# Optimization experiments

Measured on AMD Instinct MI355X. Metric: run time of the kernel, lower is better.

The kernel has to match this reference:

```python
import jax, jax.numpy as jnp
import numpy as np

B, T, D, H, L, K, DFF = 8, 512, 512, 8, 4, 31, 2048
DK = D // H
PAD = (K - 1) // 2

def _ln(x, g, b, eps=1e-5):
    m = x.mean(-1, keepdims=True)
    v = ((x - m) ** 2).mean(-1, keepdims=True)
    return (x - m) * jax.lax.rsqrt(v + eps) * g + b

def _swish(x):
    return x * jax.nn.sigmoid(x)

def _rel_shift(x):
    # x: [B,H,T,P] with P = 2T-1 (Transformer-XL style shift)
    b, h, q, p = x.shape
    x = jnp.pad(x, ((0, 0), (0, 0), (0, 0), (1, 0)))
    x = x.reshape(b, h, p + 1, q)[:, :, 1:].reshape(b, h, q, p)
    return x

def setup_inputs() -> dict:
    key = jax.random.key(0)
    ks = iter(jax.random.split(key, 64))
    def w(shape, s=0.02):
        return jax.random.normal(next(ks), shape, jnp.float32) * s
    inp = {
        'x': jax.random.normal(next(ks), (B, T, D), jnp.float32),
        'pos_emb': jax.random.normal(next(ks), (1, 2 * T - 1, D), jnp.float32),
        'ln1_g': jnp.ones((L, D)), 'ln1_b': jnp.zeros((L, D)),
        'ff1_w1': w((L, D, DFF)), 'ff1_b1': jnp.zeros((L, DFF)),
        'ff1_w2': w((L, DFF, D)), 'ff1_b2': jnp.zeros((L, D)),
        'lnA_g': jnp.ones((L, D)), 'lnA_b': jnp.zeros((L, D)),
        'Wq': w((L, D, D)), 'bq': jnp.zeros((L, D)),
        'Wk': w((L, D, D)), 'bk': jnp.zeros((L, D)),
        'Wv': w((L, D, D)), 'bv': jnp.zeros((L, D)),
        'Wo': w((L, D, D)), 'bo': jnp.zeros((L, D)),
        'Wpos': w((L, D, D)),
        'pbu': jnp.zeros((L, H, DK)), 'pbv': jnp.zeros((L, H, DK)),
        'lnC_g': jnp.ones((L, D)), 'lnC_b': jnp.zeros((L, D)),
        'pw1_w': w((L, 2 * D, D)), 'pw1_b': jnp.zeros((L, 2 * D)),
        'dw_w': w((L, D, K)), 'dw_b': jnp.zeros((L, D)),
        'cln_g': jnp.ones((L, D)), 'cln_b': jnp.zeros((L, D)),
        'pw2_w': w((L, D, D)), 'pw2_b': jnp.zeros((L, D)),
        'ln2_g': jnp.ones((L, D)), 'ln2_b': jnp.zeros((L, D)),
        'ff2_w1': w((L, D, DFF)), 'ff2_b1': jnp.zeros((L, DFF)),
        'ff2_w2': w((L, DFF, D)), 'ff2_b2': jnp.zeros((L, D)),
        'lnO_g': jnp.ones((L, D)), 'lnO_b': jnp.zeros((L, D)),
    }
    return inp

def reference(x, pos_emb, ln1_g, ln1_b, ff1_w1, ff1_b1, ff1_w2, ff1_b2,
              lnA_g, lnA_b, Wq, bq, Wk, bk, Wv, bv, Wo, bo, Wpos, pbu, pbv,
              lnC_g, lnC_b, pw1_w, pw1_b, dw_w, dw_b, cln_g, cln_b, pw2_w, pw2_b,
              ln2_g, ln2_b, ff2_w1, ff2_b1, ff2_w2, ff2_b2, lnO_g, lnO_b):
    scale = 1.0 / np.sqrt(DK).astype(np.float32)
    for i in range(L):
        # FFN 1 (half-step residual)
        res = x
        y = _ln(x, ln1_g[i], ln1_b[i])
        y = _swish(y @ ff1_w1[i] + ff1_b1[i]) @ ff1_w2[i] + ff1_b2[i]
        res = res + 0.5 * y
        # rel-pos multi-head self-attention
        y = _ln(res, lnA_g[i], lnA_b[i])
        q = (y @ Wq[i] + bq[i]).reshape(B, T, H, DK)
        k = (y @ Wk[i] + bk[i]).reshape(B, T, H, DK)
        v = (y @ Wv[i] + bv[i]).reshape(B, T, H, DK)
        p = (pos_emb @ Wpos[i]).reshape(1, 2 * T - 1, H, DK)
        ac = jnp.einsum('bthd,bshd->bhts', q + pbu[i], k)          # content score
        bd = jnp.einsum('bthd,xshd->bhts', q + pbv[i], p)          # position score
        bd = _rel_shift(bd)[..., :T]
        attn = jax.nn.softmax((ac + bd) * scale, axis=-1)
        o = jnp.einsum('bhts,bshd->bthd', attn, v).reshape(B, T, D)
        res = res + (o @ Wo[i] + bo[i])
        # convolution module
        y = _ln(res, lnC_g[i], lnC_b[i])
        y = y @ pw1_w[i].T + pw1_b[i]                               # (B,T,2D)
        a, g = jnp.split(y, 2, axis=-1)
        y = a * jax.nn.sigmoid(g)                                   # GLU over channels
        y = jax.lax.conv_general_dilated(
            y.transpose(0, 2, 1), dw_w[i][:, None, :],
            window_strides=(1,), padding=[(PAD, PAD)],
            feature_group_count=D,
            dimension_numbers=('NCH', 'OIH', 'NCH'))
        y = y.transpose(0, 2, 1) + dw_b[i]                          # (B,T,D)
        y = _swish(_ln(y, cln_g[i], cln_b[i]))
        y = y @ pw2_w[i].T + pw2_b[i]
        res = res + y
        # FFN 2 (half-step residual)
        y = _ln(res, ln2_g[i], ln2_b[i])
        y = _swish(y @ ff2_w1[i] + ff2_b1[i]) @ ff2_w2[i] + ff2_b2[i]
        res = res + 0.5 * y
        x = _ln(res, lnO_g[i], lnO_b[i])
    return x
```

## Files before the change

kernel.cpp:

```cpp
#include <hip/hip_runtime.h>


typedef unsigned short u16;
typedef unsigned int u32;
typedef __attribute__((ext_vector_type(8))) short bf16x8;
typedef __attribute__((ext_vector_type(4))) float f32x4;

#define DI __device__ __forceinline__

constexpr int CT = 512;
constexpr int CD = 512;
constexpr int CH = 8;
constexpr int CDK = 64;
constexpr int CDFF = 2048;
constexpr int CNBT = 4096;
constexpr int CL = 4;

DI u16 f2bf(float f) {
  u32 u = __builtin_bit_cast(u32, f);
  u = u + 0x7fffu + ((u >> 16) & 1u);
  return (u16)(u >> 16);
}
DI float bf2f(u16 h) { u32 u = ((u32)h) << 16; return __builtin_bit_cast(float, u); }
DI u32 pack2(float a, float b) { return (u32)f2bf(a) | ((u32)f2bf(b) << 16); }
DI float sigm(float x) { return 1.0f / (1.0f + __expf(-x)); }

DI f32x4 MFMA(bf16x8 a, bf16x8 b, f32x4 c) {
  return __builtin_amdgcn_mfma_f32_16x16x32_bf16(a, b, c, 0, 0, 0);
}

DI void gload16(const void* g, void* l) {
  __builtin_amdgcn_global_load_lds((const __attribute__((address_space(1))) void*)g,
                                   (__attribute__((address_space(3))) void*)l, 16, 0, 0);
}

DI float wsum(float v) {
#pragma unroll
  for (int o = 32; o > 0; o >>= 1) v += __shfl_xor(v, o, 64);
  return v;
}

__global__ __launch_bounds__(256) void tconv_k(const float* __restrict__ in,
                                               u16* __restrict__ out, int R, int C,
                                               long inZ, long outZ) {
  __shared__ float t[32][33];
  int c0 = blockIdx.x * 32, r0 = blockIdx.y * 32;
  const float* ip = in + (long)blockIdx.z * inZ;
  u16* op = out + (long)blockIdx.z * outZ;
#pragma unroll
  for (int i = threadIdx.y; i < 32; i += 8)
    t[i][threadIdx.x] = ip[(long)(r0 + i) * C + c0 + threadIdx.x];
  __syncthreads();
#pragma unroll
  for (int i = threadIdx.y; i < 32; i += 8)
    op[(long)(c0 + i) * R + r0 + threadIdx.x] = f2bf(t[threadIdx.x][i]);
}

__global__ __launch_bounds__(256) void cvt_k(const float* __restrict__ in,
                                             u16* __restrict__ out, long nIn, long nOut,
                                             long inZ, long outZ) {
  long i = ((long)blockIdx.x * 256 + threadIdx.x) * 4;
  if (i >= nOut) return;
  const float* ip = in + (long)blockIdx.y * inZ;
  u16* op = out + (long)blockIdx.y * outZ;
  u16 o[4];
#pragma unroll
  for (int j = 0; j < 4; ++j) {
    long idx = i + j;
    o[j] = (idx < nIn) ? f2bf(ip[idx]) : (u16)0;
  }
  uint2 st;
  st.x = (u32)o[0] | ((u32)o[1] << 16);
  st.y = (u32)o[2] | ((u32)o[3] << 16);
  *(uint2*)&op[i] = st;
}

__global__ __launch_bounds__(256) void pwperm_k(const float* __restrict__ in,
                                                u16* __restrict__ out) {
  int l = blockIdx.y;
  long i = (long)blockIdx.x * 256 + threadIdx.x;
  long n = i >> 7;
  int c = (int)(i & 127) * 4;
  int q = (int)(n >> 4) & 1;
  long r = (q ? 512 : 0) + ((n >> 5) << 4) + (n & 15);
  const float* ip = in + ((long)l * 1024 + r) * 512 + c;
  float4 v = *(const float4*)ip;
  u16* op = out + ((long)l * 1024 + n) * 512 + c;
  uint2 st;
  st.x = pack2(v.x, v.y);
  st.y = pack2(v.z, v.w);
  *(uint2*)op = st;
}

__global__ __launch_bounds__(256) void dwt_k(const float* __restrict__ in,
                                             float* __restrict__ out) {
  int l = blockIdx.y;
  int idx = blockIdx.x * 256 + threadIdx.x;
  if (idx >= 512 * 31) return;
  int k = idx >> 9, d = idx & 511;
  out[(long)l * 31 * 512 + idx] = in[(long)l * 512 * 31 + d * 31 + k];
}

__global__ __launch_bounds__(256) void qkvbias_k(const float* __restrict__ bq,
                                                 const float* __restrict__ bk,
                                                 const float* __restrict__ bv,
                                                 float* __restrict__ out) {
  int z = blockIdx.y;
  int j = blockIdx.x * 256 + threadIdx.x;
  float v;
  if (j < 512) v = bq[z * 512 + j];
  else if (j < 1024) v = bk[z * 512 + j - 512];
  else v = bv[z * 512 + j - 1024];
  out[z * 1536 + j] = v;
}

__global__ __launch_bounds__(256) void copy_k(const float* __restrict__ in,
                                              float* __restrict__ out) {
  long i = ((long)blockIdx.x * 256 + threadIdx.x) * 4;
  *(float4*)(out + i) = *(const float4*)(in + i);
}

template <int F32OUT>
__global__ __launch_bounds__(256) void ln_k(const float* in, void* out,
                                            const float* gw, const float* bw) {
  int tid = threadIdx.x, wid = tid >> 6, lane = tid & 63;
  long row = (long)blockIdx.x * 4 + wid;
  const float* x = in + row * CD + lane * 8;
  float4 v0 = *(const float4*)x;
  float4 v1 = *(const float4*)(x + 4);
  float s = v0.x + v0.y + v0.z + v0.w + v1.x + v1.y + v1.z + v1.w;
  float q = v0.x * v0.x + v0.y * v0.y + v0.z * v0.z + v0.w * v0.w +
            v1.x * v1.x + v1.y * v1.y + v1.z * v1.z + v1.w * v1.w;
  s = wsum(s);
  q = wsum(q);
  float mean = s * (1.0f / CD);
  float var = q * (1.0f / CD) - mean * mean;
  float rs = rsqrtf(var + 1e-5f);
  int c = lane * 8;
  float4 g0 = *(const float4*)(gw + c), g1 = *(const float4*)(gw + c + 4);
  float4 b0 = *(const float4*)(bw + c), b1 = *(const float4*)(bw + c + 4);
  float y0 = (v0.x - mean) * rs * g0.x + b0.x;
  float y1 = (v0.y - mean) * rs * g0.y + b0.y;
  float y2 = (v0.z - mean) * rs * g0.z + b0.z;
  float y3 = (v0.w - mean) * rs * g0.w + b0.w;
  float y4 = (v1.x - mean) * rs * g1.x + b1.x;
  float y5 = (v1.y - mean) * rs * g1.y + b1.y;
  float y6 = (v1.z - mean) * rs * g1.z + b1.z;
  float y7 = (v1.w - mean) * rs * g1.w + b1.w;
  if (F32OUT) {
    float* o = (float*)out + row * CD + c;
    *(float4*)o = make_float4(y0, y1, y2, y3);
    *(float4*)(o + 4) = make_float4(y4, y5, y6, y7);
  } else {
    u16* o = (u16*)out + row * CD + c;
    uint4 pk;
    pk.x = pack2(y0, y1);
    pk.y = pack2(y2, y3);
    pk.z = pack2(y4, y5);
    pk.w = pack2(y6, y7);
    *(uint4*)o = pk;
  }
}

template <int EPI, int SPLITK>
__global__ __launch_bounds__(256, 2) void gemm2_k(
    const u16* __restrict__ A, const u16* __restrict__ B, void* C,
    const float* __restrict__ bias, float alpha, int lda, int ldb, int ldc, int Kd) {
  __shared__ u16 lds[2][2][64 * 64];
  const int tid = threadIdx.x, wid = tid >> 6, lane = tid & 63;
  const int m0 = blockIdx.x * 64, n0 = blockIdx.y * 64;
  const int wm = wid >> 1, wn = wid & 1;
  const int fr = lane & 15, fq = lane >> 4;
  const f32x4 vz = {0.f, 0.f, 0.f, 0.f};
  f32x4 acc[2][2] = {{vz, vz}, {vz, vz}};

  const int Kc = Kd / SPLITK;
  const int kb0 = (SPLITK > 1) ? blockIdx.z * Kc : 0;
  const int nK = Kc / 64;

  auto stage = [&](int buf, int kt) {
    const int k0 = kb0 + kt * 64;
#pragma unroll
    for (int r = 0; r < 2; ++r) {
      int bi = r * 4096 + tid * 16;
      int row = bi >> 7;
      int ch = ((bi >> 4) & 7) ^ (row & 7);
      gload16(A + (long)(m0 + row) * lda + k0 + ch * 8,
              (char*)&lds[buf][0][0] + r * 4096 + wid * 1024);
      gload16(B + (long)(n0 + row) * ldb + k0 + ch * 8,
              (char*)&lds[buf][1][0] + r * 4096 + wid * 1024);
    }
  };

  stage(0, 0);
  asm volatile("s_waitcnt vmcnt(0)" ::: "memory");
  __syncthreads();
  int buf = 0;
  for (int kt = 0; kt < nK; ++kt) {
    if (kt + 1 < nK) stage(buf ^ 1, kt + 1);
    bf16x8 af[2][2], bfv[2][2];
#pragma unroll
    for (int ks = 0; ks < 2; ++ks) {
      int ch = ks * 4 + fq;
#pragma unroll
      for (int i = 0; i < 2; ++i) {
        int arow = wm * 32 + i * 16 + fr;
        af[ks][i] = *(const bf16x8*)((const char*)&lds[buf][0][0] + arow * 128 +
                                     ((ch ^ (arow & 7)) << 4));
        int brow = wn * 32 + i * 16 + fr;
        bfv[ks][i] = *(const bf16x8*)((const char*)&lds[buf][1][0] + brow * 128 +
                                      ((ch ^ (brow & 7)) << 4));
      }
    }
#pragma unroll
    for (int ks = 0; ks < 2; ++ks)
#pragma unroll
      for (int mi = 0; mi < 2; ++mi)
#pragma unroll
        for (int ni = 0; ni < 2; ++ni)
          acc[mi][ni] = MFMA(af[ks][mi], bfv[ks][ni], acc[mi][ni]);
    asm volatile("s_waitcnt vmcnt(0)" ::: "memory");
    __syncthreads();
    buf ^= 1;
  }

  if constexpr (EPI == 7) {
    const int ucol = (n0 >> 1) + wn * 16 + fr;
    float ba = bias[ucol], bg = bias[512 + ucol];
#pragma unroll
    for (int mi = 0; mi < 2; ++mi) {
      const int gmB = m0 + wm * 32 + mi * 16 + fq * 4;
#pragma unroll
      for (int r = 0; r < 4; ++r) {
        float va = acc[mi][0][r] + ba;
        float vg = acc[mi][1][r] + bg;
        ((u16*)C)[(long)(gmB + r) * 512 + ucol] = f2bf(va * sigm(vg));
      }
    }
  } else {
#pragma unroll
    for (int mi = 0; mi < 2; ++mi) {
      const int gmB = m0 + wm * 32 + mi * 16 + fq * 4;
#pragma unroll
      for (int ni = 0; ni < 2; ++ni) {
        const int gn = n0 + wn * 32 + ni * 16 + fr;
        float bv_ = 0.f;
        if constexpr (EPI == 1 || EPI == 2 || EPI == 3) bv_ = bias[gn];
#pragma unroll
        for (int r = 0; r < 4; ++r) {
          const int gm = gmB + r;
          float v = acc[mi][ni][r];
          long idx = (long)gm * ldc + gn;
          if constexpr (EPI == 0) ((u16*)C)[idx] = f2bf(v);
          else if constexpr (EPI == 1) ((u16*)C)[idx] = f2bf(v + bv_);
          else if constexpr (EPI == 2) {
            float x = v + bv_;
            ((u16*)C)[idx] = f2bf(x * sigm(x));
          } else if constexpr (EPI == 3) {
            float* R = (float*)C;
            if constexpr (SPLITK > 1) {
              float add = alpha * (v + (blockIdx.z == 0 ? bv_ : 0.f));
              atomicAdd(&R[idx], add);
            } else {
              R[idx] += alpha * (v + bv_);
            }
          }
        }
      }
    }
  }
}

__global__ __launch_bounds__(256) void vtrans_k(const u16* __restrict__ qkv,
                                                u16* __restrict__ vt) {
  __shared__ u16 t[64][80];
  int tid = threadIdx.x;
  int t0 = blockIdx.x * 64;
  int bh = blockIdx.y, b = bh >> 3, h = bh & 7;
  {
    int tl = tid >> 2, dg = (tid & 3) * 16;
    const u16* src = qkv + ((long)(b * CT + t0 + tl)) * 1536 + 1024 + h * 64 + dg;
    uint4 a0 = *(const uint4*)src;
    uint4 a1 = *(const uint4*)(src + 8);
    *(uint4*)&t[tl][dg] = a0;
    *(uint4*)&t[tl][dg + 8] = a1;
  }
  __syncthreads();
  {
    int dl = tid >> 2, tg = (tid & 3) * 16;
    u16* dst = vt + ((long)bh * 64 + dl) * CT + t0 + tg;
    u16 tmp[16];
#pragma unroll
    for (int j = 0; j < 16; ++j) tmp[j] = t[tg + j][dl];
    uint4 o0, o1;
    o0.x = (u32)tmp[0] | ((u32)tmp[1] << 16);
    o0.y = (u32)tmp[2] | ((u32)tmp[3] << 16);
    o0.z = (u32)tmp[4] | ((u32)tmp[5] << 16);
    o0.w = (u32)tmp[6] | ((u32)tmp[7] << 16);
    o1.x = (u32)tmp[8] | ((u32)tmp[9] << 16);
    o1.y = (u32)tmp[10] | ((u32)tmp[11] << 16);
    o1.z = (u32)tmp[12] | ((u32)tmp[13] << 16);
    o1.w = (u32)tmp[14] | ((u32)tmp[15] << 16);
    *(uint4*)dst = o0;
    *(uint4*)(dst + 8) = o1;
  }
}

__global__ __launch_bounds__(256, 2) void attn_k(
    const u16* __restrict__ qkvp, const u16* __restrict__ pball,
    const float* __restrict__ pbuL, const float* __restrict__ pbvL,
    const u16* __restrict__ vt, u16* __restrict__ out) {
  __shared__ u16 ldsK[2][64 * 64];
  __shared__ u16 ldsP[2][128 * 64];
  __shared__ u16 bd0s[4][16 * 80];
  __shared__ u16 stile[4][16 * 64];
  const int tid = threadIdx.x, wid = tid >> 6, lane = tid & 63;
  const int t0 = blockIdx.x * 64;
  const int bh = blockIdx.y, b = bh >> 3, h = bh & 7;
  const int fr = lane & 15, fq = lane >> 4;

  const u16* kbase = qkvp + (long)(b * CT) * 1536 + 512 + h * 64;
  const u16* pbase = pball + h * 64;
  const float* pu = pbuL + h * 64;
  const float* pv = pbvL + h * 64;

  const u16* qp = qkvp + (long)(b * CT + t0 + wid * 16 + fr) * 1536 + h * 64;
  bf16x8 qua[2], qva[2];
#pragma unroll
  for (int kk = 0; kk < 2; ++kk) {
    bf16x8 qw = *(const bf16x8*)(qp + kk * 32 + fq * 8);
    const float* bu = pu + kk * 32 + fq * 8;
    const float* bv = pv + kk * 32 + fq * 8;
#pragma unroll
    for (int j = 0; j < 8; ++j) {
      float qf = bf2f((u16)qw[j]);
      qua[kk][j] = (short)f2bf(qf + bu[j]);
      qva[kk][j] = (short)f2bf(qf + bv[j]);
    }
  }

  const f32x4 vz = {0.f, 0.f, 0.f, 0.f};
  f32x4 oacc[4] = {vz, vz, vz, vz};
  float m_run[4] = {-1e30f, -1e30f, -1e30f, -1e30f};
  float l_run[4] = {0.f, 0.f, 0.f, 0.f};
  const int jbw = (3 - wid) * 16;

  auto stage = [&](int buf, int st) {
    int s0 = st * 64, j0 = s0 - t0 + 448;
#pragma unroll
    for (int r = 0; r < 2; ++r) {
      int c = r * 256 + tid;
      int row = c >> 3, cs = (c & 7) ^ (row & 7);
      gload16(kbase + (long)(s0 + row) * 1536 + cs * 8,
              (char*)&ldsK[buf][0] + r * 4096 + wid * 1024);
    }
#pragma unroll
    for (int r = 0; r < 4; ++r) {
      int c = r * 256 + tid;
      int row = c >> 3, cs = (c & 7) ^ (row & 7);
      gload16(pbase + (long)(j0 + row) * 2048 + cs * 8,
              (char*)&ldsP[buf][0] + r * 4096 + wid * 1024);
    }
  };

  stage(0, 0);
  int cur = 0;
  for (int st = 0; st < 8; ++st) {
    const int s0 = st * 64;
    if (st + 1 < 8) {
      stage(cur ^ 1, st + 1);
      asm volatile("s_waitcnt vmcnt(6)" ::: "memory");
    } else {
      asm volatile("s_waitcnt vmcnt(0)" ::: "memory");
    }
    __syncthreads();

    bf16x8 vb[4][2];
#pragma unroll
    for (int ni = 0; ni < 4; ++ni)
#pragma unroll
      for (int kk = 0; kk < 2; ++kk)
        vb[ni][kk] = *(const bf16x8*)&vt[((long)bh * 64 + ni * 16 + fr) * 512 +
                                         s0 + kk * 32 + fq * 8];

    f32x4 ac[4] = {vz, vz, vz, vz};
#pragma unroll
    for (int kk = 0; kk < 2; ++kk) {
#pragma unroll
      for (int ni = 0; ni < 4; ++ni) {
        int row = ni * 16 + fr;
        bf16x8 kb = *(const bf16x8*)((const char*)&ldsK[cur][0] +
                                     ((row * 128 + kk * 64 + fq * 16) ^ ((row & 7) << 4)));
        ac[ni] = MFMA(qua[kk], kb, ac[ni]);
      }
    }
    f32x4 bd[5] = {vz, vz, vz, vz, vz};
#pragma unroll
    for (int kk = 0; kk < 2; ++kk) {
#pragma unroll
      for (int nbi = 0; nbi < 5; ++nbi) {
        int row = jbw + nbi * 16 + fr;
        bf16x8 pb = *(const bf16x8*)((const char*)&ldsP[cur][0] +
                                     ((row * 128 + kk * 64 + fq * 16) ^ ((row & 7) << 4)));
        bd[nbi] = MFMA(qva[kk], pb, bd[nbi]);
      }
    }
#pragma unroll
    for (int nbi = 0; nbi < 5; ++nbi)
#pragma unroll
      for (int r = 0; r < 4; ++r)
        bd0s[wid][(fq * 4 + r) * 80 + nbi * 16 + fr] = f2bf(bd[nbi][r]);

    float vals[4][4];
#pragma unroll
    for (int ni = 0; ni < 4; ++ni)
#pragma unroll
      for (int r = 0; r < 4; ++r) {
        int tlw = fq * 4 + r;
        int jcol = ni * 16 + fr + 15 - tlw;
        vals[ni][r] = (ac[ni][r] + bf2f(bd0s[wid][tlw * 80 + jcol])) * 0.125f;
      }
    float scf[4];
#pragma unroll
    for (int r = 0; r < 4; ++r) {
      float mx = fmaxf(fmaxf(vals[0][r], vals[1][r]), fmaxf(vals[2][r], vals[3][r]));
      mx = fmaxf(mx, __shfl_xor(mx, 1));
      mx = fmaxf(mx, __shfl_xor(mx, 2));
      mx = fmaxf(mx, __shfl_xor(mx, 4));
      mx = fmaxf(mx, __shfl_xor(mx, 8));
      float mnew = fmaxf(m_run[r], mx);
      scf[r] = __expf(m_run[r] - mnew);
      m_run[r] = mnew;
      float sum = 0.f;
#pragma unroll
      for (int ni = 0; ni < 4; ++ni) {
        float p = __expf(vals[ni][r] - mnew);
        vals[ni][r] = p;
        sum += p;
      }
      sum += __shfl_xor(sum, 1);
      sum += __shfl_xor(sum, 2);
      sum += __shfl_xor(sum, 4);
      sum += __shfl_xor(sum, 8);
      l_run[r] = l_run[r] * scf[r] + sum;
    }
#pragma unroll
    for (int ni = 0; ni < 4; ++ni)
#pragma unroll
      for (int r = 0; r < 4; ++r) {
        int tlw = fq * 4 + r;
        *(u16*)((char*)&stile[wid][0] +
                (((tlw * 128) + (ni * 16 + fr) * 2) ^ ((tlw & 7) << 4))) =
            f2bf(vals[ni][r]);
      }
#pragma unroll
    for (int ni = 0; ni < 4; ++ni)
#pragma unroll
      for (int r = 0; r < 4; ++r) oacc[ni][r] *= scf[r];
#pragma unroll
    for (int kk = 0; kk < 2; ++kk) {
      bf16x8 pa = *(const bf16x8*)((const char*)&stile[wid][0] +
                                   ((fr * 128 + kk * 64 + fq * 16) ^ ((fr & 7) << 4)));
#pragma unroll
      for (int ni = 0; ni < 4; ++ni) oacc[ni] = MFMA(pa, vb[ni][kk], oacc[ni]);
    }
    __syncthreads();
    cur ^= 1;
  }

  float inv[4];
#pragma unroll
  for (int r = 0; r < 4; ++r) inv[r] = 1.0f / l_run[r];
#pragma unroll
  for (int ni = 0; ni < 4; ++ni)
#pragma unroll
    for (int r = 0; r < 4; ++r) {
      long row = (long)(b * CT + t0 + wid * 16 + fq * 4 + r) * CD + h * CDK;
      out[row + ni * 16 + fr] = f2bf(oacc[ni][r] * inv[r]);
    }
}

__global__ __launch_bounds__(256) void conv2_k(const u16* __restrict__ u,
                                               const float* __restrict__ wT,
                                               const float* __restrict__ wb,
                                               const float* __restrict__ cg,
                                               const float* __restrict__ cb,
                                               u16* __restrict__ out) {
  constexpr int TT = 8;
  int tid = threadIdx.x, d0 = tid * 2;
  int b = blockIdx.y, t0 = blockIdx.x * TT;
  const u16* ub = u + ((long)b * CT) * CD + d0;

  u32 strip[TT + 30];
#pragma unroll
  for (int j = 0; j < TT + 30; ++j) {
    int tt = t0 + j - 15;
    strip[j] = ((unsigned)tt < (unsigned)CT) ? *(const u32*)(ub + (long)tt * CD) : 0u;
  }
  float2 bias = *(const float2*)(wb + d0);
  float a0[TT], a1[TT];
#pragma unroll
  for (int t = 0; t < TT; ++t) { a0[t] = bias.x; a1[t] = bias.y; }
#pragma unroll
  for (int k = 0; k < 31; ++k) {
    float2 wk = *(const float2*)(wT + k * CD + d0);
#pragma unroll
    for (int t = 0; t < TT; ++t) {
      u32 pr = strip[t + k];
      a0[t] += bf2f((u16)(pr & 0xffff)) * wk.x;
      a1[t] += bf2f((u16)(pr >> 16)) * wk.y;
    }
  }
  __shared__ float redS[4][TT], redQ[4][TT];
  int wid = tid >> 6, lane = tid & 63;
#pragma unroll
  for (int t = 0; t < TT; ++t) {
    float s = a0[t] + a1[t];
    float q = a0[t] * a0[t] + a1[t] * a1[t];
    s = wsum(s);
    q = wsum(q);
    if (lane == 0) { redS[wid][t] = s; redQ[wid][t] = q; }
  }
  __syncthreads();
  float2 g2 = *(const float2*)(cg + d0);
  float2 b2 = *(const float2*)(cb + d0);
#pragma unroll
  for (int t = 0; t < TT; ++t) {
    float s = redS[0][t] + redS[1][t] + redS[2][t] + redS[3][t];
    float q = redQ[0][t] + redQ[1][t] + redQ[2][t] + redQ[3][t];
    float mean = s * (1.f / 512), var = q * (1.f / 512) - mean * mean;
    float rs = rsqrtf(var + 1e-5f);
    float y0 = (a0[t] - mean) * rs * g2.x + b2.x;
    float y1 = (a1[t] - mean) * rs * g2.y + b2.y;
    y0 = y0 * sigm(y0);
    y1 = y1 * sigm(y1);
    *(u32*)(out + ((long)(b * CT + t0 + t)) * CD + d0) = pack2(y0, y1);
  }
}

extern "C" void kernel_launch(void* const* d_in, const int* in_sizes, int n_in,
                              void* d_out, int out_size, void* d_ws, size_t ws_size,
                              hipStream_t stream) {
  const float* in_x   = (const float*)d_in[0];
  const float* in_pos = (const float*)d_in[1];
  const float* ln1_g  = (const float*)d_in[2];
  const float* ln1_b  = (const float*)d_in[3];
  const float* ff1_w1 = (const float*)d_in[4];
  const float* ff1_b1 = (const float*)d_in[5];
  const float* ff1_w2 = (const float*)d_in[6];
  const float* ff1_b2 = (const float*)d_in[7];
  const float* lnA_g  = (const float*)d_in[8];
  const float* lnA_b  = (const float*)d_in[9];
  const float* Wq     = (const float*)d_in[10];
  const float* bq     = (const float*)d_in[11];
  const float* Wk     = (const float*)d_in[12];
  const float* bk     = (const float*)d_in[13];
  const float* Wv     = (const float*)d_in[14];
  const float* bv     = (const float*)d_in[15];
  const float* Wo     = (const float*)d_in[16];
  const float* bo     = (const float*)d_in[17];
  const float* Wpos   = (const float*)d_in[18];
  const float* pbu    = (const float*)d_in[19];
  const float* pbv    = (const float*)d_in[20];
  const float* lnC_g  = (const float*)d_in[21];
  const float* lnC_b  = (const float*)d_in[22];
  const float* pw1_w  = (const float*)d_in[23];
  const float* pw1_b  = (const float*)d_in[24];
  const float* dw_w   = (const float*)d_in[25];
  const float* dw_b   = (const float*)d_in[26];
  const float* cln_g  = (const float*)d_in[27];
  const float* cln_b  = (const float*)d_in[28];
  const float* pw2_w  = (const float*)d_in[29];
  const float* pw2_b  = (const float*)d_in[30];
  const float* ln2_g  = (const float*)d_in[31];
  const float* ln2_b  = (const float*)d_in[32];
  const float* ff2_w1 = (const float*)d_in[33];
  const float* ff2_b1 = (const float*)d_in[34];
  const float* ff2_w2 = (const float*)d_in[35];
  const float* ff2_b2 = (const float*)d_in[36];
  const float* lnO_g  = (const float*)d_in[37];
  const float* lnO_b  = (const float*)d_in[38];
  (void)in_sizes; (void)n_in; (void)out_size; (void)ws_size;

  char* ws = (char*)d_ws;
  size_t off = 0;
  auto alloc = [&](size_t bytes) -> void* {
    off = (off + 255) & ~(size_t)255;
    void* p = ws + off;
    off += bytes;
    return p;
  };

  u16* wt_ff1w1 = (u16*)alloc((size_t)CL * CDFF * CD * 2);
  u16* wt_ff1w2 = (u16*)alloc((size_t)CL * CD * CDFF * 2);
  u16* wt_qkv   = (u16*)alloc((size_t)CL * 1536 * CD * 2);
  u16* wt_o     = (u16*)alloc((size_t)CL * CD * CD * 2);
  u16* wt_pos   = (u16*)alloc((size_t)CL * CD * CD * 2);
  u16* w_pw1p   = (u16*)alloc((size_t)CL * 1024 * CD * 2);
  u16* w_pw2    = (u16*)alloc((size_t)CL * CD * CD * 2);
  u16* wt_ff2w1 = (u16*)alloc((size_t)CL * CDFF * CD * 2);
  u16* wt_ff2w2 = (u16*)alloc((size_t)CL * CD * CDFF * 2);
  float* qkvbias = (float*)alloc((size_t)CL * 1536 * 4);
  u16* posbf = (u16*)alloc((size_t)1024 * CD * 2);
  float* dwT = (float*)alloc((size_t)CL * 31 * CD * 4);
  u16* pbf_all = (u16*)alloc((size_t)1024 * 2048 * 2);
  float* cur = (float*)alloc((size_t)CNBT * CD * 4);
  u16* ybf   = (u16*)alloc((size_t)CNBT * CD * 2);
  u16* qkv   = (u16*)alloc((size_t)CNBT * 1536 * 2);
  u16* hbf   = (u16*)alloc((size_t)CNBT * CDFF * 2);
  u16* vt    = (u16*)alloc((size_t)64 * CDK * CT * 2);
  u16* obf   = (u16*)alloc((size_t)CNBT * CD * 2);
  u16* ubuf  = (u16*)alloc((size_t)CNBT * CD * 2);
  u16* cbf   = (u16*)alloc((size_t)CNBT * CD * 2);

  dim3 b256(256);
  dim3 tb(32, 8);

  tconv_k<<<dim3(CDFF / 32, CD / 32, CL), tb, 0, stream>>>(ff1_w1, wt_ff1w1, CD, CDFF,
                                                           (long)CD * CDFF, (long)CDFF * CD);
  tconv_k<<<dim3(CD / 32, CDFF / 32, CL), tb, 0, stream>>>(ff1_w2, wt_ff1w2, CDFF, CD,
                                                           (long)CDFF * CD, (long)CD * CDFF);
  tconv_k<<<dim3(CD / 32, CD / 32, CL), tb, 0, stream>>>(Wq, wt_qkv, CD, CD,
                                                         (long)CD * CD, 1536L * CD);
  tconv_k<<<dim3(CD / 32, CD / 32, CL), tb, 0, stream>>>(Wk, wt_qkv + 512 * 512, CD, CD,
                                                         (long)CD * CD, 1536L * CD);
  tconv_k<<<dim3(CD / 32, CD / 32, CL), tb, 0, stream>>>(Wv, wt_qkv + 1024 * 512, CD, CD,
                                                         (long)CD * CD, 1536L * CD);
  tconv_k<<<dim3(CD / 32, CD / 32, CL), tb, 0, stream>>>(Wo, wt_o, CD, CD,
                                                         (long)CD * CD, (long)CD * CD);
  tconv_k<<<dim3(CD / 32, CD / 32, CL), tb, 0, stream>>>(Wpos, wt_pos, CD, CD,
                                                         (long)CD * CD, (long)CD * CD);
  tconv_k<<<dim3(CDFF / 32, CD / 32, CL), tb, 0, stream>>>(ff2_w1, wt_ff2w1, CD, CDFF,
                                                           (long)CD * CDFF, (long)CDFF * CD);
  tconv_k<<<dim3(CD / 32, CDFF / 32, CL), tb, 0, stream>>>(ff2_w2, wt_ff2w2, CDFF, CD,
                                                           (long)CDFF * CD, (long)CD * CDFF);
  pwperm_k<<<dim3(512, CL), b256, 0, stream>>>(pw1_w, w_pw1p);
  cvt_k<<<dim3(256, CL, 1), b256, 0, stream>>>(pw2_w, w_pw2, 512L * 512, 512L * 512,
                                               512L * 512, 512L * 512);
  cvt_k<<<dim3(512, 1, 1), b256, 0, stream>>>(in_pos, posbf, 1023L * 512, 1024L * 512, 0, 0);
  dwt_k<<<dim3(62, CL), b256, 0, stream>>>(dw_w, dwT);
  qkvbias_k<<<dim3(6, CL), b256, 0, stream>>>(bq, bk, bv, qkvbias);
  copy_k<<<dim3(2048), b256, 0, stream>>>(in_x, cur);
  gemm2_k<0, 1><<<dim3(16, 32, 1), b256, 0, stream>>>(
      posbf, wt_pos, pbf_all, nullptr, 0.f, CD, CD, 2048, CD);

  for (int i = 0; i < CL; ++i) {
    const u16* Wf1 = wt_ff1w1 + (long)i * CDFF * CD;
    const u16* Wf2 = wt_ff1w2 + (long)i * CD * CDFF;
    const u16* Wqk = wt_qkv + (long)i * 1536 * CD;
    const u16* Wou = wt_o + (long)i * CD * CD;
    const u16* Wp1 = w_pw1p + (long)i * 1024 * CD;
    const u16* Wp2 = w_pw2 + (long)i * CD * CD;
    const u16* Wf3 = wt_ff2w1 + (long)i * CDFF * CD;
    const u16* Wf4 = wt_ff2w2 + (long)i * CD * CDFF;

    ln_k<0><<<dim3(1024), b256, 0, stream>>>(cur, ybf, ln1_g + i * CD, ln1_b + i * CD);
    gemm2_k<2, 1><<<dim3(64, 32, 1), b256, 0, stream>>>(
        ybf, Wf1, hbf, ff1_b1 + (long)i * CDFF, 0.f, CD, CD, CDFF, CD);
    gemm2_k<3, 2><<<dim3(64, 8, 2), b256, 0, stream>>>(
        hbf, Wf2, cur, ff1_b2 + i * CD, 0.5f, CDFF, CDFF, CD, CDFF);

    ln_k<0><<<dim3(1024), b256, 0, stream>>>(cur, ybf, lnA_g + i * CD, lnA_b + i * CD);
    gemm2_k<1, 1><<<dim3(64, 24, 1), b256, 0, stream>>>(
        ybf, Wqk, qkv, qkvbias + i * 1536, 0.f, CD, CD, 1536, CD);
    vtrans_k<<<dim3(8, 64), b256, 0, stream>>>(qkv, vt);
    attn_k<<<dim3(8, 64), b256, 0, stream>>>(qkv, pbf_all + i * 512, pbu + i * 512,
                                             pbv + i * 512, vt, obf);
    gemm2_k<3, 1><<<dim3(64, 8, 1), b256, 0, stream>>>(
        obf, Wou, cur, bo + i * CD, 1.0f, CD, CD, CD, CD);

    ln_k<0><<<dim3(1024), b256, 0, stream>>>(cur, ybf, lnC_g + i * CD, lnC_b + i * CD);
    gemm2_k<7, 1><<<dim3(64, 16, 1), b256, 0, stream>>>(
        ybf, Wp1, ubuf, pw1_b + (long)i * 1024, 0.f, CD, CD, 512, CD);
    conv2_k<<<dim3(CT / 8, 8), b256, 0, stream>>>(ubuf, dwT + (long)i * 31 * CD,
                                                  dw_b + i * CD, cln_g + i * CD,
                                                  cln_b + i * CD, cbf);
    gemm2_k<3, 1><<<dim3(64, 8, 1), b256, 0, stream>>>(
        cbf, Wp2, cur, pw2_b + i * CD, 1.0f, CD, CD, CD, CD);

    ln_k<0><<<dim3(1024), b256, 0, stream>>>(cur, ybf, ln2_g + i * CD, ln2_b + i * CD);
    gemm2_k<2, 1><<<dim3(64, 32, 1), b256, 0, stream>>>(
        ybf, Wf3, hbf, ff2_b1 + (long)i * CDFF, 0.f, CD, CD, CDFF, CD);
    gemm2_k<3, 2><<<dim3(64, 8, 2), b256, 0, stream>>>(
        hbf, Wf4, cur, ff2_b2 + i * CD, 0.5f, CDFF, CDFF, CD, CDFF);

    if (i < CL - 1)
      ln_k<1><<<dim3(1024), b256, 0, stream>>>(cur, cur, lnO_g + i * CD, lnO_b + i * CD);
    else
      ln_k<1><<<dim3(1024), b256, 0, stream>>>(cur, d_out, lnO_g + i * CD, lnO_b + i * CD);
  }
}
```

Baseline: 816.5 us.

## Enlarge GEMM tile to 128x64, fuse layer-end LNs, batch weight transposes

The GEMM kernel now computes 128x64 output tiles: each wave holds a 64x32 sub-tile, so more MFMAs run per LDS fragment load, and launch bounds allow three blocks per CU. The two back-to-back layer norms at a layer boundary (lnO, then the next layer's ln1) are merged into one kernel. The nine weight-transpose launches are folded into three. The Wo and pw2 projections switch to split-K of 2, which restores grid size now that tiles are larger but relies on split-K accumulation into the residual being correct. Larger tiles halve the block count and raise register pressure, which could reduce occupancy.

After: 892.9 us. 1.09x slower.

```diff
diff --git a/kernel.cpp b/kernel.cpp
--- a/kernel.cpp
+++ b/kernel.cpp
@@ -40,20 +40,48 @@
   return v;
 }
 
-__global__ __launch_bounds__(256) void tconv_k(const float* __restrict__ in,
-                                               u16* __restrict__ out, int R, int C,
-                                               long inZ, long outZ) {
+DI void tbody(const float* ip, u16* op, int R, int C, int c0, int r0,
+              int tx, int ty) {
   __shared__ float t[32][33];
-  int c0 = blockIdx.x * 32, r0 = blockIdx.y * 32;
-  const float* ip = in + (long)blockIdx.z * inZ;
-  u16* op = out + (long)blockIdx.z * outZ;
-#pragma unroll
-  for (int i = threadIdx.y; i < 32; i += 8)
-    t[i][threadIdx.x] = ip[(long)(r0 + i) * C + c0 + threadIdx.x];
+#pragma unroll
+  for (int i = ty; i < 32; i += 8)
+    t[i][tx] = ip[(long)(r0 + i) * C + c0 + tx];
   __syncthreads();
 #pragma unroll
-  for (int i = threadIdx.y; i < 32; i += 8)
-    op[(long)(c0 + i) * R + r0 + threadIdx.x] = f2bf(t[threadIdx.x][i]);
+  for (int i = ty; i < 32; i += 8)
+    op[(long)(c0 + i) * R + r0 + tx] = f2bf(t[tx][i]);
+}
+
+__global__ __launch_bounds__(256) void tconv2x_k(const float* __restrict__ in0,
+                                                 const float* __restrict__ in1,
+                                                 u16* __restrict__ out0,
+                                                 u16* __restrict__ out1,
+                                                 int R, int C) {
+  int z = blockIdx.z;
+  int l = z & 3;
+  const float* ip = (z < 4 ? in0 : in1) + (long)l * R * C;
+  u16* op = (z < 4 ? out0 : out1) + (long)l * R * C;
+  tbody(ip, op, R, C, blockIdx.x * 32, blockIdx.y * 32, threadIdx.x, threadIdx.y);
+}
+
+__global__ __launch_bounds__(256) void tconvQ_k(
+    const float* __restrict__ Wq, const float* __restrict__ Wk,
+    const float* __restrict__ Wv, const float* __restrict__ Wo,
+    const float* __restrict__ Wpos, u16* __restrict__ wt_qkv,
+    u16* __restrict__ wt_o, u16* __restrict__ wt_pos) {
+  int z = blockIdx.z;
+  int sel = z >> 2, l = z & 3;
+  const float* ip;
+  u16* op;
+  const long S = 512L * 512;
+  switch (sel) {
+    case 0: ip = Wq + l * S; op = wt_qkv + (long)l * 1536 * 512; break;
+    case 1: ip = Wk + l * S; op = wt_qkv + (long)l * 1536 * 512 + S; break;
+    case 2: ip = Wv + l * S; op = wt_qkv + (long)l * 1536 * 512 + 2 * S; break;
+    case 3: ip = Wo + l * S; op = wt_o + l * S; break;
+    default: ip = Wpos + l * S; op = wt_pos + l * S; break;
+  }
+  tbody(ip, op, 512, 512, blockIdx.x * 32, blockIdx.y * 32, threadIdx.x, threadIdx.y);
 }
 
 __global__ __launch_bounds__(256) void cvt_k(const float* __restrict__ in,
@@ -162,17 +190,61 @@
   }
 }
 
+__global__ __launch_bounds__(256) void lnln_k(float* cur, u16* ybf,
+                                              const float* gO, const float* bO,
+                                              const float* g1, const float* b1) {
+  int tid = threadIdx.x, wid = tid >> 6, lane = tid & 63;
+  long row = (long)blockIdx.x * 4 + wid;
+  float* x = cur + row * CD + lane * 8;
+  float v[8];
+  *(float4*)&v[0] = *(const float4*)x;
+  *(float4*)&v[4] = *(const float4*)(x + 4);
+  float s = 0.f, q = 0.f;
+#pragma unroll
+  for (int j = 0; j < 8; ++j) { s += v[j]; q += v[j] * v[j]; }
+  s = wsum(s);
+  q = wsum(q);
+  float mean = s * (1.0f / CD);
+  float var = q * (1.0f / CD) - mean * mean;
+  float rs = rsqrtf(var + 1e-5f);
+  int c = lane * 8;
+  float y[8];
+#pragma unroll
+  for (int j = 0; j < 8; ++j) y[j] = (v[j] - mean) * rs * gO[c + j] + bO[c + j];
+  *(float4*)x = *(float4*)&y[0];
+  *(float4*)(x + 4) = *(float4*)&y[4];
+  float s2 = 0.f, q2 = 0.f;
+#pragma unroll
+  for (int j = 0; j < 8; ++j) { s2 += y[j]; q2 += y[j] * y[j]; }
+  s2 = wsum(s2);
+  q2 = wsum(q2);
+  float mean2 = s2 * (1.0f / CD);
+  float var2 = q2 * (1.0f / CD) - mean2 * mean2;
+  float rs2 = rsqrtf(var2 + 1e-5f);
+  float z[8];
+#pragma unroll
+  for (int j = 0; j < 8; ++j) z[j] = (y[j] - mean2) * rs2 * g1[c + j] + b1[c + j];
+  u16* o = ybf + row * CD + c;
+  uint4 pk;
+  pk.x = pack2(z[0], z[1]);
+  pk.y = pack2(z[2], z[3]);
+  pk.z = pack2(z[4], z[5]);
+  pk.w = pack2(z[6], z[7]);
+  *(uint4*)o = pk;
+}
+
 template <int EPI, int SPLITK>
-__global__ __launch_bounds__(256, 2) void gemm2_k(
+__global__ __launch_bounds__(256, 3) void gemm3_k(
     const u16* __restrict__ A, const u16* __restrict__ B, void* C,
     const float* __restrict__ bias, float alpha, int lda, int ldb, int ldc, int Kd) {
-  __shared__ u16 lds[2][2][64 * 64];
+  __shared__ u16 ldsA[2][128 * 64];
+  __shared__ u16 ldsB[2][64 * 64];
   const int tid = threadIdx.x, wid = tid >> 6, lane = tid & 63;
-  const int m0 = blockIdx.x * 64, n0 = blockIdx.y * 64;
+  const int m0 = blockIdx.x * 128, n0 = blockIdx.y * 64;
   const int wm = wid >> 1, wn = wid & 1;
   const int fr = lane & 15, fq = lane >> 4;
   const f32x4 vz = {0.f, 0.f, 0.f, 0.f};
-  f32x4 acc[2][2] = {{vz, vz}, {vz, vz}};
+  f32x4 acc[4][2] = {{vz, vz}, {vz, vz}, {vz, vz}, {vz, vz}};
 
   const int Kc = Kd / SPLITK;
   const int kb0 = (SPLITK > 1) ? blockIdx.z * Kc : 0;
@@ -180,15 +252,21 @@
 
   auto stage = [&](int buf, int kt) {
     const int k0 = kb0 + kt * 64;
+#pragma unroll
+    for (int r = 0; r < 4; ++r) {
+      int bi = r * 4096 + tid * 16;
+      int row = bi >> 7;
+      int ch = ((bi >> 4) & 7) ^ (row & 7);
+      gload16(A + (long)(m0 + row) * lda + k0 + ch * 8,
+              (char*)&ldsA[buf][0] + r * 4096 + wid * 1024);
+    }
 #pragma unroll
     for (int r = 0; r < 2; ++r) {
       int bi = r * 4096 + tid * 16;
       int row = bi >> 7;
       int ch = ((bi >> 4) & 7) ^ (row & 7);
-      gload16(A + (long)(m0 + row) * lda + k0 + ch * 8,
-              (char*)&lds[buf][0][0] + r * 4096 + wid * 1024);
       gload16(B + (long)(n0 + row) * ldb + k0 + ch * 8,
-              (char*)&lds[buf][1][0] + r * 4096 + wid * 1024);
+              (char*)&ldsB[buf][0] + r * 4096 + wid * 1024);
     }
   };
 
@@ -198,27 +276,28 @@
   int buf = 0;
   for (int kt = 0; kt < nK; ++kt) {
     if (kt + 1 < nK) stage(buf ^ 1, kt + 1);
-    bf16x8 af[2][2], bfv[2][2];
 #pragma unroll
     for (int ks = 0; ks < 2; ++ks) {
       int ch = ks * 4 + fq;
+      bf16x8 af[4], bfv[2];
+#pragma unroll
+      for (int i = 0; i < 4; ++i) {
+        int arow = wm * 64 + i * 16 + fr;
+        af[i] = *(const bf16x8*)((const char*)&ldsA[buf][0] + arow * 128 +
+                                 ((ch ^ (arow & 7)) << 4));
+      }
 #pragma unroll
       for (int i = 0; i < 2; ++i) {
-        int arow = wm * 32 + i * 16 + fr;
-        af[ks][i] = *(const bf16x8*)((const char*)&lds[buf][0][0] + arow * 128 +
-                                     ((ch ^ (arow & 7)) << 4));
         int brow = wn * 32 + i * 16 + fr;
-        bfv[ks][i] = *(const bf16x8*)((const char*)&lds[buf][1][0] + brow * 128 +
-                                      ((ch ^ (brow & 7)) << 4));
-      }
-    }
-#pragma unroll
-    for (int ks = 0; ks < 2; ++ks)
-#pragma unroll
-      for (int mi = 0; mi < 2; ++mi)
+        bfv[i] = *(const bf16x8*)((const char*)&ldsB[buf][0] + brow * 128 +
+                                  ((ch ^ (brow & 7)) << 4));
+      }
+#pragma unroll
+      for (int mi = 0; mi < 4; ++mi)
 #pragma unroll
         for (int ni = 0; ni < 2; ++ni)
-          acc[mi][ni] = MFMA(af[ks][mi], bfv[ks][ni], acc[mi][ni]);
+          acc[mi][ni] = MFMA(af[mi], bfv[ni], acc[mi][ni]);
+    }
     asm volatile("s_waitcnt vmcnt(0)" ::: "memory");
     __syncthreads();
     buf ^= 1;
@@ -228,8 +307,8 @@
     const int ucol = (n0 >> 1) + wn * 16 + fr;
     float ba = bias[ucol], bg = bias[512 + ucol];
 #pragma unroll
-    for (int mi = 0; mi < 2; ++mi) {
-      const int gmB = m0 + wm * 32 + mi * 16 + fq * 4;
+    for (int mi = 0; mi < 4; ++mi) {
+      const int gmB = m0 + wm * 64 + mi * 16 + fq * 4;
 #pragma unroll
       for (int r = 0; r < 4; ++r) {
         float va = acc[mi][0][r] + ba;
@@ -239,8 +318,8 @@
     }
   } else {
 #pragma unroll
-    for (int mi = 0; mi < 2; ++mi) {
-      const int gmB = m0 + wm * 32 + mi * 16 + fq * 4;
+    for (int mi = 0; mi < 4; ++mi) {
+      const int gmB = m0 + wm * 64 + mi * 16 + fq * 4;
 #pragma unroll
       for (int ni = 0; ni < 2; ++ni) {
         const int gn = n0 + wn * 32 + ni * 16 + fr;
@@ -616,24 +695,12 @@
   dim3 b256(256);
   dim3 tb(32, 8);
 
-  tconv_k<<<dim3(CDFF / 32, CD / 32, CL), tb, 0, stream>>>(ff1_w1, wt_ff1w1, CD, CDFF,
-                                                           (long)CD * CDFF, (long)CDFF * CD);
-  tconv_k<<<dim3(CD / 32, CDFF / 32, CL), tb, 0, stream>>>(ff1_w2, wt_ff1w2, CDFF, CD,
-                                                           (long)CDFF * CD, (long)CD * CDFF);
-  tconv_k<<<dim3(CD / 32, CD / 32, CL), tb, 0, stream>>>(Wq, wt_qkv, CD, CD,
-                                                         (long)CD * CD, 1536L * CD);
-  tconv_k<<<dim3(CD / 32, CD / 32, CL), tb, 0, stream>>>(Wk, wt_qkv + 512 * 512, CD, CD,
-                                                         (long)CD * CD, 1536L * CD);
-  tconv_k<<<dim3(CD / 32, CD / 32, CL), tb, 0, stream>>>(Wv, wt_qkv + 1024 * 512, CD, CD,
-                                                         (long)CD * CD, 1536L * CD);
-  tconv_k<<<dim3(CD / 32, CD / 32, CL), tb, 0, stream>>>(Wo, wt_o, CD, CD,
-                                                         (long)CD * CD, (long)CD * CD);
-  tconv_k<<<dim3(CD / 32, CD / 32, CL), tb, 0, stream>>>(Wpos, wt_pos, CD, CD,
-                                                         (long)CD * CD, (long)CD * CD);
-  tconv_k<<<dim3(CDFF / 32, CD / 32, CL), tb, 0, stream>>>(ff2_w1, wt_ff2w1, CD, CDFF,
-                                                           (long)CD * CDFF, (long)CDFF * CD);
-  tconv_k<<<dim3(CD / 32, CDFF / 32, CL), tb, 0, stream>>>(ff2_w2, wt_ff2w2, CDFF, CD,
-                                                           (long)CDFF * CD, (long)CD * CDFF);
+  tconv2x_k<<<dim3(CDFF / 32, CD / 32, 2 * CL), tb, 0, stream>>>(
+      ff1_w1, ff2_w1, wt_ff1w1, wt_ff2w1, CD, CDFF);
+  tconv2x_k<<<dim3(CD / 32, CDFF / 32, 2 * CL), tb, 0, stream>>>(
+      ff1_w2, ff2_w2, wt_ff1w2, wt_ff2w2, CDFF, CD);
+  tconvQ_k<<<dim3(CD / 32, CD / 32, 5 * CL), tb, 0, stream>>>(
+      Wq, Wk, Wv, Wo, Wpos, wt_qkv, wt_o, wt_pos);
   pwperm_k<<<dim3(512, CL), b256, 0, stream>>>(pw1_w, w_pw1p);
   cvt_k<<<dim3(256, CL, 1), b256, 0, stream>>>(pw2_w, w_pw2, 512L * 512, 512L * 512,
                                                512L * 512, 512L * 512);
@@ -641,8 +708,9 @@
   dwt_k<<<dim3(62, CL), b256, 0, stream>>>(dw_w, dwT);
   qkvbias_k<<<dim3(6, CL), b256, 0, stream>>>(bq, bk, bv, qkvbias);
   copy_k<<<dim3(2048), b256, 0, stream>>>(in_x, cur);
-  gemm2_k<0, 1><<<dim3(16, 32, 1), b256, 0, stream>>>(
+  gemm3_k<0, 1><<<dim3(8, 32, 1), b256, 0, stream>>>(
       posbf, wt_pos, pbf_all, nullptr, 0.f, CD, CD, 2048, CD);
+  ln_k<0><<<dim3(1024), b256, 0, stream>>>(cur, ybf, ln1_g, ln1_b);
 
   for (int i = 0; i < CL; ++i) {
     const u16* Wf1 = wt_ff1w1 + (long)i * CDFF * CD;
@@ -654,38 +722,38 @@
     const u16* Wf3 = wt_ff2w1 + (long)i * CDFF * CD;
     const u16* Wf4 = wt_ff2w2 + (long)i * CD * CDFF;
 
-    ln_k<0><<<dim3(1024), b256, 0, stream>>>(cur, ybf, ln1_g + i * CD, ln1_b + i * CD);
-    gemm2_k<2, 1><<<dim3(64, 32, 1), b256, 0, stream>>>(
+    gemm3_k<2, 1><<<dim3(32, 32, 1), b256, 0, stream>>>(
         ybf, Wf1, hbf, ff1_b1 + (long)i * CDFF, 0.f, CD, CD, CDFF, CD);
-    gemm2_k<3, 2><<<dim3(64, 8, 2), b256, 0, stream>>>(
+    gemm3_k<3, 2><<<dim3(32, 8, 2), b256, 0, stream>>>(
         hbf, Wf2, cur, ff1_b2 + i * CD, 0.5f, CDFF, CDFF, CD, CDFF);
 
     ln_k<0><<<dim3(1024), b256, 0, stream>>>(cur, ybf, lnA_g + i * CD, lnA_b + i * CD);
-    gemm2_k<1, 1><<<dim3(64, 24, 1), b256, 0, stream>>>(
+    gemm3_k<1, 1><<<dim3(32, 24, 1), b256, 0, stream>>>(
         ybf, Wqk, qkv, qkvbias + i * 1536, 0.f, CD, CD, 1536, CD);
     vtrans_k<<<dim3(8, 64), b256, 0, stream>>>(qkv, vt);
     attn_k<<<dim3(8, 64), b256, 0, stream>>>(qkv, pbf_all + i * 512, pbu + i * 512,
                                              pbv + i * 512, vt, obf);
-    gemm2_k<3, 1><<<dim3(64, 8, 1), b256, 0, stream>>>(
+    gemm3_k<3, 2><<<dim3(32, 8, 2), b256, 0, stream>>>(
         obf, Wou, cur, bo + i * CD, 1.0f, CD, CD, CD, CD);
 
     ln_k<0><<<dim3(1024), b256, 0, stream>>>(cur, ybf, lnC_g + i * CD, lnC_b + i * CD);
-    gemm2_k<7, 1><<<dim3(64, 16, 1), b256, 0, stream>>>(
+    gemm3_k<7, 1><<<dim3(32, 16, 1), b256, 0, stream>>>(
         ybf, Wp1, ubuf, pw1_b + (long)i * 1024, 0.f, CD, CD, 512, CD);
     conv2_k<<<dim3(CT / 8, 8), b256, 0, stream>>>(ubuf, dwT + (long)i * 31 * CD,
                                                   dw_b + i * CD, cln_g + i * CD,
                                                   cln_b + i * CD, cbf);
-    gemm2_k<3, 1><<<dim3(64, 8, 1), b256, 0, stream>>>(
+    gemm3_k<3, 2><<<dim3(32, 8, 2), b256, 0, stream>>>(
         cbf, Wp2, cur, pw2_b + i * CD, 1.0f, CD, CD, CD, CD);
 
     ln_k<0><<<dim3(1024), b256, 0, stream>>>(cur, ybf, ln2_g + i * CD, ln2_b + i * CD);
-    gemm2_k<2, 1><<<dim3(64, 32, 1), b256, 0, stream>>>(
+    gemm3_k<2, 1><<<dim3(32, 32, 1), b256, 0, stream>>>(
         ybf, Wf3, hbf, ff2_b1 + (long)i * CDFF, 0.f, CD, CD, CDFF, CD);
-    gemm2_k<3, 2><<<dim3(64, 8, 2), b256, 0, stream>>>(
+    gemm3_k<3, 2><<<dim3(32, 8, 2), b256, 0, stream>>>(
         hbf, Wf4, cur, ff2_b2 + i * CD, 0.5f, CDFF, CDFF, CD, CDFF);
 
     if (i < CL - 1)
-      ln_k<1><<<dim3(1024), b256, 0, stream>>>(cur, cur, lnO_g + i * CD, lnO_b + i * CD);
+      lnln_k<<<dim3(1024), b256, 0, stream>>>(cur, ybf, lnO_g + i * CD, lnO_b + i * CD,
+                                              ln1_g + (i + 1) * CD, ln1_b + (i + 1) * CD);
     else
       ln_k<1><<<dim3(1024), b256, 0, stream>>>(cur, d_out, lnO_g + i * CD, lnO_b + i * CD);
   }
```
